# Kernel optimization log

Measured on AMD Instinct MI355X. Metric: run time of the kernel, lower is better.

Reference implementation:

```python
import jax, jax.numpy as jnp
import numpy as np

N_NODES = 16384
N_EDGES = 131072
EDGE_DIM = 16
IN_CH = 32
OUT_CH = 32
HID_EDGE = 64
MLP_HID = 64  # int(32 * 2.0)
OUT_FINAL = 10
N_GRAPHS = 64
BN_EPS = 1e-5


def setup_inputs() -> dict:
    key = jax.random.key(0)
    ks = jax.random.split(key, 20)
    s = lambda *sh: 1.0 / np.sqrt(sh[0])
    inp = {
        'x': jax.random.normal(ks[0], (N_NODES, IN_CH), jnp.float32),
        'edge_attr': jax.random.normal(ks[1], (N_EDGES, EDGE_DIM), jnp.float32),
        'edge_index': jax.random.randint(ks[2], (2, N_EDGES), 0, N_NODES, jnp.int64),
        'batch': jnp.sort(jax.random.randint(ks[3], (N_NODES,), 0, N_GRAPHS, jnp.int64)),
    }
    # layer 0: edge MLP (EDGE_DIM->HID_EDGE->IN_CH*OUT_CH), root, bias, BN affine
    inp['w1_0'] = jax.random.normal(ks[4], (EDGE_DIM, HID_EDGE), jnp.float32) * s(EDGE_DIM)
    inp['b1_0'] = jnp.zeros((HID_EDGE,), jnp.float32)
    inp['w2_0'] = jax.random.normal(ks[5], (HID_EDGE, IN_CH * OUT_CH), jnp.float32) * s(HID_EDGE)
    inp['b2_0'] = jnp.zeros((IN_CH * OUT_CH,), jnp.float32)
    inp['root_0'] = jax.random.normal(ks[6], (IN_CH, OUT_CH), jnp.float32) * s(IN_CH)
    inp['bias_0'] = jnp.zeros((OUT_CH,), jnp.float32)
    inp['gamma_0'] = jnp.ones((OUT_CH,), jnp.float32)
    inp['beta_0'] = jnp.zeros((OUT_CH,), jnp.float32)
    # layer 1: edge MLP (EDGE_DIM->HID_EDGE->OUT_CH*OUT_CH)
    inp['w1_1'] = jax.random.normal(ks[7], (EDGE_DIM, HID_EDGE), jnp.float32) * s(EDGE_DIM)
    inp['b1_1'] = jnp.zeros((HID_EDGE,), jnp.float32)
    inp['w2_1'] = jax.random.normal(ks[8], (HID_EDGE, OUT_CH * OUT_CH), jnp.float32) * s(HID_EDGE)
    inp['b2_1'] = jnp.zeros((OUT_CH * OUT_CH,), jnp.float32)
    inp['root_1'] = jax.random.normal(ks[9], (OUT_CH, OUT_CH), jnp.float32) * s(OUT_CH)
    inp['bias_1'] = jnp.zeros((OUT_CH,), jnp.float32)
    inp['gamma_1'] = jnp.ones((OUT_CH,), jnp.float32)
    inp['beta_1'] = jnp.zeros((OUT_CH,), jnp.float32)
    # final MLP (dropout is identity in eval / deterministic reference)
    inp['mlp_w1'] = jax.random.normal(ks[10], (OUT_CH, MLP_HID), jnp.float32) * s(OUT_CH)
    inp['mlp_b1'] = jnp.zeros((MLP_HID,), jnp.float32)
    inp['mlp_w2'] = jax.random.normal(ks[11], (MLP_HID, OUT_FINAL), jnp.float32) * s(MLP_HID)
    inp['mlp_b2'] = jnp.zeros((OUT_FINAL,), jnp.float32)
    return inp


def _nnconv(x, src, dst, edge_attr, w1, b1, w2, b2, root, bias, out_ch):
    # per-edge weight matrices from the edge MLP: [E, in, out]
    h = jax.nn.relu(edge_attr @ w1 + b1)
    W = (h @ w2 + b2).reshape(-1, x.shape[1], out_ch)
    msg = jnp.einsum('ei,eio->eo', x[src], W)  # gather + per-edge matmul
    agg = jax.ops.segment_sum(msg, dst, num_segments=N_NODES)
    cnt = jax.ops.segment_sum(jnp.ones((dst.shape[0], 1), x.dtype), dst, num_segments=N_NODES)
    agg = agg / jnp.maximum(cnt, 1.0)  # scatter-mean (zero-degree nodes -> 0)
    return agg + x @ root + bias


def _bn(x, gamma, beta):
    m = jnp.mean(x, axis=0)
    v = jnp.var(x, axis=0)
    return (x - m) * jax.lax.rsqrt(v + BN_EPS) * gamma + beta


def reference(x, edge_attr, edge_index, batch,
              w1_0, b1_0, w2_0, b2_0, root_0, bias_0, gamma_0, beta_0,
              w1_1, b1_1, w2_1, b2_1, root_1, bias_1, gamma_1, beta_1,
              mlp_w1, mlp_b1, mlp_w2, mlp_b2):
    src, dst = edge_index[0], edge_index[1]
    h = _nnconv(x, src, dst, edge_attr, w1_0, b1_0, w2_0, b2_0, root_0, bias_0, OUT_CH)
    h = jax.nn.relu(_bn(h, gamma_0, beta_0))
    h = _nnconv(h, src, dst, edge_attr, w1_1, b1_1, w2_1, b2_1, root_1, bias_1, OUT_CH)
    h = jax.nn.relu(_bn(h, gamma_1, beta_1))
    # global mean pool over graphs
    pooled = jax.ops.segment_sum(h, batch, num_segments=N_GRAPHS)
    gcnt = jax.ops.segment_sum(jnp.ones((h.shape[0], 1), h.dtype), batch, num_segments=N_GRAPHS)
    pooled = pooled / jnp.maximum(gcnt, 1.0)
    logits = jax.nn.relu(pooled @ mlp_w1 + mlp_b1) @ mlp_w2 + mlp_b2
    return logits
```

## Files before the change

kernel.cpp:

```cpp
#include <hip/hip_runtime.h>
#include <hip/hip_bf16.h>

#define NN 16384
#define NE 131072
#define NG 64
#define EPB 128

typedef unsigned short u16;
typedef unsigned int u32;
typedef __attribute__((ext_vector_type(8))) short short8;
typedef __attribute__((ext_vector_type(4))) float f32x4;
typedef __attribute__((ext_vector_type(2))) float f32x2;
typedef __attribute__((ext_vector_type(8))) _Float16 f16x8;
typedef __attribute__((ext_vector_type(2))) _Float16 f16x2;
typedef __attribute__((address_space(1))) const unsigned int gu32;
typedef __attribute__((address_space(3))) unsigned int lu32;

__device__ __forceinline__ float bf2f(u16 u) {
    u32 x = ((u32)u) << 16;
    return __builtin_bit_cast(float, x);
}
__device__ __forceinline__ u16 f2bf(float f) {
    u32 u = __builtin_bit_cast(u32, f);
    u = u + 0x7fffu + ((u >> 16) & 1u);
    return (u16)(u >> 16);
}
__device__ __forceinline__ u16 f2h(float f) {
    _Float16 h = (_Float16)f;
    return __builtin_bit_cast(u16, h);
}
__device__ __forceinline__ f16x2 pkrtz(float a, float b) {
    auto v = __builtin_amdgcn_cvt_pkrtz(a, b);
    static_assert(sizeof(v) == 4, "pkrtz size");
    return __builtin_bit_cast(f16x2, v);
}
#if __has_builtin(__builtin_amdgcn_cvt_pk_bf16_f32)
__device__ __forceinline__ u32 pk2bf_fast(float a, float b) {
    auto v = __builtin_amdgcn_cvt_pk_bf16_f32(a, b);
    static_assert(sizeof(v) == 4, "cvt_pk_bf16 size");
    return __builtin_bit_cast(u32, v);
}
#else
__device__ __forceinline__ u32 pk2bf_fast(float a, float b) {
    u32 ua = __builtin_bit_cast(u32, a) + 0x8000u;
    u32 ub = __builtin_bit_cast(u32, b) + 0x8000u;
    return __builtin_amdgcn_perm(ub, ua, 0x07060302u);
}
#endif
__device__ __forceinline__ float loadF(const void* p, int i, bool bf) {
    return bf ? bf2f(((const u16*)p)[i]) : ((const float*)p)[i];
}
__device__ __forceinline__ int loadI(const void* p, int i, bool i64) {
    return i64 ? (int)((const long long*)p)[i] : ((const int*)p)[i];
}
__device__ __forceinline__ bool det_bf(const void* g0) {
    return ((const u16*)g0)[0] == 0x3F80u;
}
__device__ __forceinline__ bool det_i64(const void* eidx) {
    const u32* u = (const u32*)eidx;
    return (u[1] | u[3] | u[5] | u[7]) == 0u;
}

__global__ __launch_bounds__(256) void k_prep(const void* w2a, const void* b2a,
                                              const void* w2b, const void* b2b,
                                              const void* w1a, const void* w1b,
                                              u16* bp0, u16* bp1, u16* w1p0, u16* w1p1,
                                              const void* eidx, float* cnt, const void* g0) {
    const bool bf = det_bf(g0);
    int id = blockIdx.x * 256 + threadIdx.x;
    if (id < 2 * 66560) {
        int l = id / 66560, v = id % 66560;
        int j = v & 7, lane = (v >> 3) & 63, nt = (v >> 9) & 1, t = v >> 10;
        int kk = (lane >> 4) * 8 + j;
        int n = (lane & 15) + 16 * nt;
        const void* w2 = l ? w2b : w2a;
        const void* b2 = l ? b2b : b2a;
        float val = (t < 64) ? loadF(w2, t * 1024 + kk * 32 + n, bf)
                             : loadF(b2, kk * 32 + n, bf);
        (l ? bp1 : bp0)[v] = f2h(val);
    } else if (id < 2 * 66560 + 2 * 2048) {
        int v = id - 2 * 66560;
        int l = v >> 11; v &= 2047;
        int j = v & 7, lane = (v >> 3) & 63, nt = v >> 9;
        int k = (lane >> 4) * 8 + j;
        int n = nt * 16 + (lane & 15);
        const void* w1 = l ? w1b : w1a;
        float val = (k < 16) ? loadF(w1, k * 64 + n, bf) : 0.f;
        (l ? w1p1 : w1p0)[v] = f2bf(val);
    } else {
        const bool i64 = det_i64(eidx);
        int e = id - (2 * 66560 + 2 * 2048);
        int d = loadI(eidx, NE + e, i64);
        atomicAdd(&cnt[d], 1.0f);
    }
}

__device__ __forceinline__ void stage_chunk(const u16* Bpack, u16* lds, int cc, int w, int lane) {
    const char* src = (const char*)Bpack + (size_t)cc * 8192 + (size_t)(w * 1024 + lane * 16);
    char* dst = (char*)lds + w * 1024;
    __builtin_amdgcn_global_load_lds((gu32*)src, (lu32*)dst, 16, 0, 0);
}

#define HSTR 72
__global__ __launch_bounds__(512, 8) void k_edge(const void* ea, const u16* w1p, const void* b1,
                                                 const void* xv, int layer1,
                                                 const float* sSp, const float* sQp,
                                                 const void* gammap, const void* betap,
                                                 const void* eidx, const u16* Bpack,
                                                 float* agg, const void* g0) {
    const bool bf = det_bf(g0);
    const bool i64 = det_i64(eidx);
    __shared__ __align__(16) u16 hl[EPB * HSTR];
    __shared__ __align__(16) u16 Bls[2][4096];
    __shared__ __align__(16) float bnS[32], bnB[32];
    const int tid = threadIdx.x;
    const int e0 = blockIdx.x * EPB;
    const int lane = tid & 63;
    const int w = tid >> 6;
    const int q = lane >> 4;
    const int m = lane & 15;
    const int wbl = w * 16;
    const int wb = e0 + wbl;

    stage_chunk(Bpack, Bls[0], 0, w, lane);
    stage_chunk(Bpack, Bls[1], 1, w, lane);

    if (layer1 && tid < 32) {
        float s = 0.f, qq = 0.f;
#pragma unroll
        for (int p = 0; p < 16; p++) { s += sSp[p * 32 + tid]; qq += sQp[p * 32 + tid]; }
        float mn = s * (1.0f / 16384.0f);
        float var = qq * (1.0f / 16384.0f) - mn * mn;
        float inv = rsqrtf(var + 1e-5f);
        float g = loadF(gammap, tid, bf), b = loadF(betap, tid, bf);
        bnS[tid] = inv * g;
        bnB[tid] = b - mn * inv * g;
    }

    {
        short8 Ah;
        {
            int eg = wb + m;
            uint4 av = make_uint4(0u, 0u, 0u, 0u);
            if (bf) {
                uint4 t = *(const uint4*)((const char*)ea + (size_t)eg * 32 + (q & 1) * 16);
                if (q < 2) av = t;
            } else {
                const float4* p = (const float4*)((const char*)ea + (size_t)eg * 64 + (q & 1) * 32);
                float4 a = p[0], b = p[1];
                if (q < 2) av = make_uint4(pk2bf_fast(a.x, a.y), pk2bf_fast(a.z, a.w),
                                           pk2bf_fast(b.x, b.y), pk2bf_fast(b.z, b.w));
            }
            Ah = __builtin_bit_cast(short8, av);
        }
#pragma unroll
        for (int nt = 0; nt < 4; nt++) {
            uint4 bw = *(const uint4*)&w1p[(nt * 64 + lane) * 8];
            short8 Bf = __builtin_bit_cast(short8, bw);
            float bb = loadF(b1, nt * 16 + m, bf);
            f32x4 c = __builtin_amdgcn_mfma_f32_16x16x32_bf16(
                Ah, Bf, f32x4{0.f, 0.f, 0.f, 0.f}, 0, 0, 0);
            int rbase = (wbl + q * 4) * HSTR + nt * 16 + m;
#pragma unroll
            for (int r = 0; r < 4; r++) {
                _Float16 hv = (_Float16)fmaxf(c[r] + bb, 0.f);
                hl[rbase + r * HSTR] = __builtin_bit_cast(u16, hv);
            }
        }
    }

    float4 ga, gb;
    {
        int s = loadI(eidx, wb + m, i64);
        if (layer1 || !bf) {
            const float4* xp = (const float4*)xv + (size_t)s * 8 + q * 2;
            ga = xp[0]; gb = xp[1];
        } else {
            const uint4* xp = (const uint4*)((const char*)xv + (size_t)s * 64 + q * 16);
            uint4 a = *xp;
            ga = make_float4(bf2f((u16)(a.x & 0xffff)), bf2f((u16)(a.x >> 16)),
                             bf2f((u16)(a.y & 0xffff)), bf2f((u16)(a.y >> 16)));
            gb = make_float4(bf2f((u16)(a.z & 0xffff)), bf2f((u16)(a.z >> 16)),
                             bf2f((u16)(a.w & 0xffff)), bf2f((u16)(a.w >> 16)));
        }
    }

    __syncthreads();

    f16x2 xh[4];
    if (layer1) {
        float4 s0 = *(const float4*)&bnS[q * 8], s1 = *(const float4*)&bnS[q * 8 + 4];
        float4 h0 = *(const float4*)&bnB[q * 8], h1 = *(const float4*)&bnB[q * 8 + 4];
        xh[0] = pkrtz(fmaxf(ga.x * s0.x + h0.x, 0.f), fmaxf(ga.y * s0.y + h0.y, 0.f));
        xh[1] = pkrtz(fmaxf(ga.z * s0.z + h0.z, 0.f), fmaxf(ga.w * s0.w + h0.w, 0.f));
        xh[2] = pkrtz(fmaxf(gb.x * s1.x + h1.x, 0.f), fmaxf(gb.y * s1.y + h1.y, 0.f));
        xh[3] = pkrtz(fmaxf(gb.z * s1.z + h1.z, 0.f), fmaxf(gb.w * s1.w + h1.w, 0.f));
    } else {
        xh[0] = pkrtz(ga.x, ga.y);
        xh[1] = pkrtz(ga.z, ga.w);
        xh[2] = pkrtz(gb.x, gb.y);
        xh[3] = pkrtz(gb.z, gb.w);
    }

    f32x4 acc0 = f32x4{0.f, 0.f, 0.f, 0.f};
    f32x4 acc1 = f32x4{0.f, 0.f, 0.f, 0.f};
    const int rowb = (wbl + m) * HSTR;

    for (int cc = 0; cc < 16; cc++) {
        uint2 hw = *(const uint2*)&hl[rowb + cc * 4];
        const u16* Bb = &Bls[cc & 1][lane * 8];
#pragma unroll
        for (int tt = 0; tt < 4; tt++) {
            uint4 bu0 = *(const uint4*)(Bb + (tt * 2 + 0) * 512);
            uint4 bu1 = *(const uint4*)(Bb + (tt * 2 + 1) * 512);
            f16x8 B0 = __builtin_bit_cast(f16x8, bu0);
            f16x8 B1 = __builtin_bit_cast(f16x8, bu1);
            const u32 sel = (tt & 1) ? 0x03020302u : 0x01000100u;
            u32 wd = (tt & 2) ? hw.y : hw.x;
            u32 hh = __builtin_amdgcn_perm(wd, wd, sel);
            f16x2 h2 = __builtin_bit_cast(f16x2, hh);
            f16x2 p0 = h2 * xh[0];
            f16x2 p1 = h2 * xh[1];
            f16x2 p2 = h2 * xh[2];
            f16x2 p3 = h2 * xh[3];
            uint4 au = make_uint4(__builtin_bit_cast(u32, p0), __builtin_bit_cast(u32, p1),
                                  __builtin_bit_cast(u32, p2), __builtin_bit_cast(u32, p3));
            f16x8 A = __builtin_bit_cast(f16x8, au);
            acc0 = __builtin_amdgcn_mfma_f32_16x16x32_f16(A, B0, acc0, 0, 0, 0);
            acc1 = __builtin_amdgcn_mfma_f32_16x16x32_f16(A, B1, acc1, 0, 0, 0);
        }
        __syncthreads();
        if (cc < 15) stage_chunk(Bpack, Bls[cc & 1], cc + 2, w, lane);
    }
    {
        const u16* Bb = &Bls[0][lane * 8];
        uint4 bu0 = *(const uint4*)(Bb + 0);
        uint4 bu1 = *(const uint4*)(Bb + 512);
        f16x8 B0 = __builtin_bit_cast(f16x8, bu0);
        f16x8 B1 = __builtin_bit_cast(f16x8, bu1);
        uint4 au = make_uint4(__builtin_bit_cast(u32, xh[0]), __builtin_bit_cast(u32, xh[1]),
                              __builtin_bit_cast(u32, xh[2]), __builtin_bit_cast(u32, xh[3]));
        f16x8 A = __builtin_bit_cast(f16x8, au);
        acc0 = __builtin_amdgcn_mfma_f32_16x16x32_f16(A, B0, acc0, 0, 0, 0);
        acc1 = __builtin_amdgcn_mfma_f32_16x16x32_f16(A, B1, acc1, 0, 0, 0);
    }

    {
        int eb = wb + q * 4;
#pragma unroll
        for (int r = 0; r < 4; r++) {
            int dst = loadI(eidx, NE + eb + r, i64);
            float* ap = agg + (size_t)dst * 32 + m;
            atomicAdd(ap, acc0[r]);
            atomicAdd(ap + 16, acc1[r]);
        }
    }
}

__global__ __launch_bounds__(256) void k_node(float* agg, const float* cnt,
                                              const void* xv, int layer1,
                                              const float* sSp, const float* sQp,
                                              const void* gammap, const void* betap,
                                              const void* root, const void* bias,
                                              float* hpre, float* sS, float* sQ,
                                              const void* g0) {
    const bool bf = det_bf(g0);
    const int tid = threadIdx.x;
    const int v = blockIdx.x * 8 + (tid >> 5);
    const int o = tid & 31;
    __shared__ float bnS[32], bnB[32];
    if (layer1) {
        if (tid < 32) {
            float s = 0.f, qq = 0.f;
#pragma unroll
            for (int p = 0; p < 16; p++) { s += sSp[p * 32 + tid]; qq += sQp[p * 32 + tid]; }
            float mn = s * (1.0f / 16384.0f);
            float var = qq * (1.0f / 16384.0f) - mn * mn;
            float inv = rsqrtf(var + 1e-5f);
            float g = loadF(gammap, tid, bf), b = loadF(betap, tid, bf);
            bnS[tid] = inv * g;
            bnB[tid] = b - mn * inv * g;
        }
        __syncthreads();
    }
    float xrow[32];
    if (layer1) {
        const float* x = (const float*)xv + (size_t)v * 32;
#pragma unroll
        for (int i = 0; i < 32; i++) xrow[i] = fmaxf(x[i] * bnS[i] + bnB[i], 0.f);
    } else if (!bf) {
        const float* x = (const float*)xv + (size_t)v * 32;
#pragma unroll
        for (int i = 0; i < 32; i++) xrow[i] = x[i];
    } else {
        const u16* x = (const u16*)xv + (size_t)v * 32;
#pragma unroll
        for (int i = 0; i < 32; i++) xrow[i] = bf2f(x[i]);
    }
    float a;
    if (bf) {
        const u16* R = (const u16*)root;
        a = bf2f(((const u16*)bias)[o]);
#pragma unroll
        for (int i = 0; i < 32; i++) a += xrow[i] * bf2f(R[i * 32 + o]);
    } else {
        const float* R = (const float*)root;
        a = ((const float*)bias)[o];
#pragma unroll
        for (int i = 0; i < 32; i++) a += xrow[i] * R[i * 32 + o];
    }
    float av = agg[(size_t)v * 32 + o];
    agg[(size_t)v * 32 + o] = 0.f;
    float pre = av / fmaxf(cnt[v], 1.0f) + a;
    hpre[(size_t)v * 32 + o] = pre;

    __shared__ float lS[256], lQ[256];
    lS[tid] = pre;
    lQ[tid] = pre * pre;
    __syncthreads();
#pragma unroll
    for (int off = 128; off >= 32; off >>= 1) {
        if (tid < off) { lS[tid] += lS[tid + off]; lQ[tid] += lQ[tid + off]; }
        __syncthreads();
    }
    if (tid < 32) {
        int slot = (blockIdx.x & 15) * 32 + tid;
        atomicAdd(&sS[slot], lS[tid]);
        atomicAdd(&sQ[slot], lQ[tid]);
    }
}

__global__ __launch_bounds__(256) void k_bnpool(const float* hpre, const float* sS, const float* sQ,
                                                const void* gamma, const void* beta,
                                                const void* batch, float* pooled, float* gcnt,
                                                const void* eidx, const void* g0) {
    const bool bf = det_bf(g0);
    const bool i64 = det_i64(eidx);
    const int tid = threadIdx.x;
    const int o = tid & 31;
    const int c = tid >> 5;
    float s = 0.f, qq = 0.f;
#pragma unroll
    for (int p = 0; p < 16; p++) { s += sS[p * 32 + o]; qq += sQ[p * 32 + o]; }
    float mn = s * (1.0f / 16384.0f);
    float var = qq * (1.0f / 16384.0f) - mn * mn;
    float inv = rsqrtf(var + 1e-5f);
    float gg = loadF(gamma, o, bf), bb = loadF(beta, o, bf);

    const int base = blockIdx.x * 256 + c;
    float acc = 0.f, cacc = 0.f;
    int curg = -1;
#pragma unroll 4
    for (int j = 0; j < 32; j++) {
        int v = base + j * 8;
        int g = loadI(batch, v, i64);
        float y = fmaxf((hpre[(size_t)v * 32 + o] - mn) * inv * gg + bb, 0.f);
        if (g != curg) {
            if (curg >= 0) {
                atomicAdd(&pooled[curg * 32 + o], acc);
                if (o == 0) atomicAdd(&gcnt[curg], cacc);
            }
            acc = 0.f; cacc = 0.f; curg = g;
        }
        acc += y; cacc += 1.f;
    }
    if (curg >= 0) {
        atomicAdd(&pooled[curg * 32 + o], acc);
        if (o == 0) atomicAdd(&gcnt[curg], cacc);
    }
}

__global__ __launch_bounds__(64) void k_final(const float* pooled, const float* gcnt,
                        const void* w1, const void* b1, const void* w2, const void* b2,
                        void* out, const void* g0) {
    const bool bf = det_bf(g0);
    const int g = blockIdx.x;
    const int j = threadIdx.x;
    float inv = 1.0f / fmaxf(gcnt[g], 1.0f);
    float a = loadF(b1, j, bf);
#pragma unroll
    for (int i = 0; i < 32; i++) {
        float p = pooled[g * 32 + i] * inv;
        a += p * loadF(w1, i * 64 + j, bf);
    }
    a = fmaxf(a, 0.f);
    float lg[10];
#pragma unroll
    for (int c = 0; c < 10; c++) lg[c] = a * loadF(w2, j * 10 + c, bf);
#pragma unroll
    for (int off = 32; off >= 1; off >>= 1) {
#pragma unroll
        for (int c = 0; c < 10; c++) lg[c] += __shfl_down(lg[c], off, 64);
    }
    if (j == 0) {
        if (bf) {
            u16* op = (u16*)out;
#pragma unroll
            for (int c = 0; c < 10; c++) op[g * 10 + c] = f2bf(lg[c] + loadF(b2, c, bf));
        } else {
            float* op = (float*)out;
#pragma unroll
            for (int c = 0; c < 10; c++) op[g * 10 + c] = lg[c] + loadF(b2, c, bf);
        }
    }
}

extern "C" void kernel_launch(void* const* d_in, const int* in_sizes, int n_in,
                              void* d_out, int out_size, void* d_ws, size_t ws_size,
                              hipStream_t stream) {
    char* ws = (char*)d_ws;
    u16* bp0  = (u16*)(ws + 256);
    u16* bp1  = (u16*)(ws + 256 + 133120);
    u16* w1p0 = (u16*)(ws + 266496);
    u16* w1p1 = (u16*)(ws + 270592);
    char* zbase = ws + 274688;
    float* agg    = (float*)(zbase);
    float* cnt    = (float*)(zbase + 2097152);
    float* sS0    = (float*)(zbase + 2162688);
    float* sQ0    = (float*)(zbase + 2164736);
    float* sS1    = (float*)(zbase + 2166784);
    float* sQ1    = (float*)(zbase + 2168832);
    float* pooled = (float*)(zbase + 2170880);
    float* gcnt   = (float*)(zbase + 2179072);
    const size_t zsize = 2179328;
    float* hpre0 = (float*)(ws + 274688 + 2179328);
    float* hpre1 = (float*)(ws + 274688 + 2179328 + 2097152);

    const void* x     = d_in[0];
    const void* ea    = d_in[1];
    const void* eidx  = d_in[2];
    const void* batch = d_in[3];
    const void* g0    = d_in[10];

    (void)hipMemsetAsync(zbase, 0, zsize, stream);
    k_prep<<<1048, 256, 0, stream>>>(d_in[6], d_in[7], d_in[14], d_in[15],
                                     d_in[4], d_in[12],
                                     bp0, bp1, w1p0, w1p1, eidx, cnt, g0);

    k_edge<<<NE / EPB, 512, 0, stream>>>(ea, w1p0, d_in[5], x, 0,
                                         nullptr, nullptr, nullptr, nullptr,
                                         eidx, bp0, agg, g0);
    k_node<<<NN / 8, 256, 0, stream>>>(agg, cnt, x, 0,
                                       nullptr, nullptr, nullptr, nullptr,
                                       d_in[8], d_in[9], hpre0, sS0, sQ0, g0);

    k_edge<<<NE / EPB, 512, 0, stream>>>(ea, w1p1, d_in[13], hpre0, 1,
                                         sS0, sQ0, d_in[10], d_in[11],
                                         eidx, bp1, agg, g0);
    k_node<<<NN / 8, 256, 0, stream>>>(agg, cnt, hpre0, 1,
                                       sS0, sQ0, d_in[10], d_in[11],
                                       d_in[16], d_in[17], hpre1, sS1, sQ1, g0);

    k_bnpool<<<NN / 256, 256, 0, stream>>>(hpre1, sS1, sQ1, d_in[18], d_in[19], batch,
                                           pooled, gcnt, eidx, g0);
    k_final<<<NG, 64, 0, stream>>>(pooled, gcnt, d_in[20], d_in[21], d_in[22], d_in[23], d_out, g0);
}
```

Before: 209.9 us.

## Replace atomic scatter with per-node edge lists and gather reduction

The edge kernel now writes per-edge messages to a dense buffer instead of atomically adding into per-node accumulators. The prep kernel builds per-destination edge lists (capped at 64 entries) from the atomic counter's return value, and the node kernel gathers and sums the messages for its node. This removes float atomics and the agg zeroing, but adds a 16 MB message write plus a random gather read per layer. Nodes with more than 64 incoming edges would be silently truncated, and the summation order is nondeterministic.

```diff
diff --git a/kernel.cpp b/kernel.cpp
--- a/kernel.cpp
+++ b/kernel.cpp
@@ -65,7 +65,8 @@
                                               const void* w2b, const void* b2b,
                                               const void* w1a, const void* w1b,
                                               u16* bp0, u16* bp1, u16* w1p0, u16* w1p1,
-                                              const void* eidx, float* cnt, const void* g0) {
+                                              const void* eidx, float* cnt, u32* eord,
+                                              const void* g0) {
     const bool bf = det_bf(g0);
     int id = blockIdx.x * 256 + threadIdx.x;
     if (id < 2 * 66560) {
@@ -91,7 +92,8 @@
         const bool i64 = det_i64(eidx);
         int e = id - (2 * 66560 + 2 * 2048);
         int d = loadI(eidx, NE + e, i64);
-        atomicAdd(&cnt[d], 1.0f);
+        int slot = (int)atomicAdd(&cnt[d], 1.0f);
+        if (slot < 64) eord[d * 64 + slot] = (u32)e;
     }
 }
 
@@ -107,7 +109,7 @@
                                                  const float* sSp, const float* sQp,
                                                  const void* gammap, const void* betap,
                                                  const void* eidx, const u16* Bpack,
-                                                 float* agg, const void* g0) {
+                                                 float* msg, const void* g0) {
     const bool bf = det_bf(g0);
     const bool i64 = det_i64(eidx);
     __shared__ __align__(16) u16 hl[EPB * HSTR];
@@ -246,18 +248,16 @@
     }
 
     {
-        int eb = wb + q * 4;
+        float* mp = msg + (size_t)(wb + q * 4) * 32 + m;
 #pragma unroll
         for (int r = 0; r < 4; r++) {
-            int dst = loadI(eidx, NE + eb + r, i64);
-            float* ap = agg + (size_t)dst * 32 + m;
-            atomicAdd(ap, acc0[r]);
-            atomicAdd(ap + 16, acc1[r]);
-        }
-    }
-}
-
-__global__ __launch_bounds__(256) void k_node(float* agg, const float* cnt,
+            mp[r * 32] = acc0[r];
+            mp[r * 32 + 16] = acc1[r];
+        }
+    }
+}
+
+__global__ __launch_bounds__(256) void k_node(const float* msg, const u32* eord, const float* cnt,
                                               const void* xv, int layer1,
                                               const float* sSp, const float* sQp,
                                               const void* gammap, const void* betap,
@@ -309,9 +309,18 @@
 #pragma unroll
         for (int i = 0; i < 32; i++) a += xrow[i] * R[i * 32 + o];
     }
-    float av = agg[(size_t)v * 32 + o];
-    agg[(size_t)v * 32 + o] = 0.f;
-    float pre = av / fmaxf(cnt[v], 1.0f) + a;
+    int deg = (int)cnt[v];
+    if (deg > 64) deg = 64;
+    const u32* ep = eord + (size_t)v * 64;
+    float av0 = 0.f, av1 = 0.f;
+    int j = 0;
+    for (; j + 1 < deg; j += 2) {
+        u32 ea0 = ep[j], ea1 = ep[j + 1];
+        av0 += msg[(size_t)ea0 * 32 + o];
+        av1 += msg[(size_t)ea1 * 32 + o];
+    }
+    if (j < deg) av0 += msg[(size_t)ep[j] * 32 + o];
+    float pre = (av0 + av1) / fmaxf(cnt[v], 1.0f) + a;
     hpre[(size_t)v * 32 + o] = pre;
 
     __shared__ float lS[256], lQ[256];
@@ -414,17 +423,19 @@
     u16* w1p0 = (u16*)(ws + 266496);
     u16* w1p1 = (u16*)(ws + 270592);
     char* zbase = ws + 274688;
-    float* agg    = (float*)(zbase);
-    float* cnt    = (float*)(zbase + 2097152);
-    float* sS0    = (float*)(zbase + 2162688);
-    float* sQ0    = (float*)(zbase + 2164736);
-    float* sS1    = (float*)(zbase + 2166784);
-    float* sQ1    = (float*)(zbase + 2168832);
-    float* pooled = (float*)(zbase + 2170880);
-    float* gcnt   = (float*)(zbase + 2179072);
-    const size_t zsize = 2179328;
-    float* hpre0 = (float*)(ws + 274688 + 2179328);
-    float* hpre1 = (float*)(ws + 274688 + 2179328 + 2097152);
+    float* cnt    = (float*)(zbase);
+    float* sS0    = (float*)(zbase + 65536);
+    float* sQ0    = (float*)(zbase + 67584);
+    float* sS1    = (float*)(zbase + 69632);
+    float* sQ1    = (float*)(zbase + 71680);
+    float* pooled = (float*)(zbase + 73728);
+    float* gcnt   = (float*)(zbase + 81920);
+    const size_t zsize = 82176;
+    char* nz = zbase + 82176;
+    u32*   eord  = (u32*)(nz);
+    float* msg   = (float*)(nz + 4194304);
+    float* hpre0 = (float*)(nz + 4194304 + 16777216);
+    float* hpre1 = (float*)(nz + 4194304 + 16777216 + 2097152);
 
     const void* x     = d_in[0];
     const void* ea    = d_in[1];
@@ -435,19 +446,19 @@
     (void)hipMemsetAsync(zbase, 0, zsize, stream);
     k_prep<<<1048, 256, 0, stream>>>(d_in[6], d_in[7], d_in[14], d_in[15],
                                      d_in[4], d_in[12],
-                                     bp0, bp1, w1p0, w1p1, eidx, cnt, g0);
+                                     bp0, bp1, w1p0, w1p1, eidx, cnt, eord, g0);
 
     k_edge<<<NE / EPB, 512, 0, stream>>>(ea, w1p0, d_in[5], x, 0,
                                          nullptr, nullptr, nullptr, nullptr,
-                                         eidx, bp0, agg, g0);
-    k_node<<<NN / 8, 256, 0, stream>>>(agg, cnt, x, 0,
+                                         eidx, bp0, msg, g0);
+    k_node<<<NN / 8, 256, 0, stream>>>(msg, eord, cnt, x, 0,
                                        nullptr, nullptr, nullptr, nullptr,
                                        d_in[8], d_in[9], hpre0, sS0, sQ0, g0);
 
     k_edge<<<NE / EPB, 512, 0, stream>>>(ea, w1p1, d_in[13], hpre0, 1,
                                          sS0, sQ0, d_in[10], d_in[11],
-                                         eidx, bp1, agg, g0);
-    k_node<<<NN / 8, 256, 0, stream>>>(agg, cnt, hpre0, 1,
+                                         eidx, bp1, msg, g0);
+    k_node<<<NN / 8, 256, 0, stream>>>(msg, eord, cnt, hpre0, 1,
                                        sS0, sQ0, d_in[10], d_in[11],
                                        d_in[16], d_in[17], hpre1, sS1, sQ1, g0);
 
```

After: 214.6 us. +2.3%, slower.
